# Performance work log

Hardware: AMD Instinct MI355X
Metric: run time of the kernel (lower is better)

Reference implementation:

```python
import jax, jax.numpy as jnp
import numpy as np

B, N, H = 16, 4096, 2048

def setup_inputs() -> dict:
    key = jax.random.key(0)
    k1, k2 = jax.random.split(key)
    outputs = jax.random.normal(k1, (B, N, H), dtype=jnp.float32)
    last_h = jax.random.normal(k2, (B, H), dtype=jnp.float32)
    return {"outputs": outputs, "last_h": last_h}

def reference(outputs, last_h):
    # q: [B, H] single query; k = v = outputs: [B, N, H]
    scale = jnp.asarray(outputs.shape[-1] ** 0.5, dtype=outputs.dtype)
    # logits: [B, N]
    logits = jnp.einsum("bh,bnh->bn", last_h, outputs) / scale
    attn = jax.nn.softmax(logits, axis=-1)          # [B, N]
    ctx = jnp.einsum("bn,bnh->bh", attn, outputs)   # [B, H]
    return (ctx, attn)
```

## Files before the change

### kernel.cpp

```cpp
#include <hip/hip_runtime.h>
#include <math.h>

constexpr int B = 16;
constexpr int N = 4096;
constexpr int H = 2048;

constexpr int BLOCKS_PER_BATCH = 64;
constexpr int WAVES_PER_BLOCK  = 4;
constexpr int WAVES_PER_BATCH  = BLOCKS_PER_BATCH * WAVES_PER_BLOCK;
constexpr int ROWS_PER_WAVE    = N / WAVES_PER_BATCH;
constexpr int F4_PER_ROW       = H / 4;
constexpr int F4_PER_LANE      = F4_PER_ROW / 64;

constexpr float kInvScale = 0.022097086912079608f;

__global__ __launch_bounds__(256, 4) void attn_pass1(
    const float* __restrict__ outs,
    const float* __restrict__ last_h,
    float* __restrict__ ws_logits,
    float* __restrict__ ws_m,
    float* __restrict__ ws_l,
    float* __restrict__ ws_ctx)
{
    const int b    = blockIdx.x / BLOCKS_PER_BATCH;
    const int blk  = blockIdx.x % BLOCKS_PER_BATCH;
    const int wave = threadIdx.x >> 6;
    const int lane = threadIdx.x & 63;
    const int wid  = blk * WAVES_PER_BLOCK + wave;
    const int row0 = wid * ROWS_PER_WAVE;

    const float4* q4 = reinterpret_cast<const float4*>(last_h + (size_t)b * H);
    float4 q[F4_PER_LANE];
#pragma unroll
    for (int j = 0; j < F4_PER_LANE; ++j) q[j] = q4[lane + 64 * j];

    float4 ctx[F4_PER_LANE];
#pragma unroll
    for (int j = 0; j < F4_PER_LANE; ++j) ctx[j] = make_float4(0.f, 0.f, 0.f, 0.f);
    float m = -INFINITY;
    float l = 0.f;

    const float4* krow = reinterpret_cast<const float4*>(outs) +
                         ((size_t)b * N + row0) * F4_PER_ROW;

    for (int r = 0; r < ROWS_PER_WAVE; ++r) {
        float4 k[F4_PER_LANE];
#pragma unroll
        for (int j = 0; j < F4_PER_LANE; ++j) k[j] = krow[lane + 64 * j];
        krow += F4_PER_ROW;

        float s = 0.f;
#pragma unroll
        for (int j = 0; j < F4_PER_LANE; ++j)
            s += k[j].x * q[j].x + k[j].y * q[j].y + k[j].z * q[j].z + k[j].w * q[j].w;
#pragma unroll
        for (int off = 32; off > 0; off >>= 1) s += __shfl_xor(s, off, 64);
        s *= kInvScale;

        if (lane == 0) ws_logits[(size_t)b * N + row0 + r] = s;

        if (s > m) {
            const float corr = __expf(m - s);
            l *= corr;
#pragma unroll
            for (int j = 0; j < F4_PER_LANE; ++j) {
                ctx[j].x *= corr; ctx[j].y *= corr;
                ctx[j].z *= corr; ctx[j].w *= corr;
            }
            m = s;
        }
        const float w = __expf(s - m);
        l += w;
#pragma unroll
        for (int j = 0; j < F4_PER_LANE; ++j) {
            ctx[j].x += w * k[j].x; ctx[j].y += w * k[j].y;
            ctx[j].z += w * k[j].z; ctx[j].w += w * k[j].w;
        }
    }

    const int gw = b * WAVES_PER_BATCH + wid;
    if (lane == 0) { ws_m[gw] = m; ws_l[gw] = l; }
    float4* cdst = reinterpret_cast<float4*>(ws_ctx) + (size_t)gw * F4_PER_ROW;
#pragma unroll
    for (int j = 0; j < F4_PER_LANE; ++j) cdst[lane + 64 * j] = ctx[j];
}

__global__ __launch_bounds__(256) void attn_pass2(
    const float* __restrict__ ws_logits,
    const float* __restrict__ ws_m,
    const float* __restrict__ ws_l,
    const float* __restrict__ ws_ctx,
    float* __restrict__ out_ctx,
    float* __restrict__ out_attn)
{
    __shared__ float lm[WAVES_PER_BATCH];
    __shared__ float lscale[WAVES_PER_BATCH];
    __shared__ float lsl[WAVES_PER_BATCH];
    __shared__ float4 red[128];

    const int bid  = blockIdx.x;
    const int b    = bid >> 3;
    const int part = bid & 7;
    const int tid  = threadIdx.x;

    const float mw = ws_m[b * WAVES_PER_BATCH + tid];
    const float lw = ws_l[b * WAVES_PER_BATCH + tid];
    lm[tid] = mw;
    __syncthreads();

    float M = -INFINITY;
    for (int w = 0; w < WAVES_PER_BATCH; ++w) M = fmaxf(M, lm[w]);

    const float sc = __expf(mw - M);
    lscale[tid] = sc;
    lsl[tid]    = sc * lw;
    __syncthreads();

    float L = 0.f;
    for (int w = 0; w < WAVES_PER_BATCH; ++w) L += lsl[w];
    const float invL = 1.f / L;

    if (part < 4) {
        const int f  = part * 128 + (tid & 127);
        const int wh = tid >> 7;
        const float4* c4 = reinterpret_cast<const float4*>(ws_ctx) +
                           (size_t)b * WAVES_PER_BATCH * F4_PER_ROW;
        float4 acc = make_float4(0.f, 0.f, 0.f, 0.f);
        for (int w = wh * 128; w < wh * 128 + 128; ++w) {
            const float s = lscale[w];
            const float4 v = c4[(size_t)w * F4_PER_ROW + f];
            acc.x += s * v.x; acc.y += s * v.y;
            acc.z += s * v.z; acc.w += s * v.w;
        }
        if (wh == 1) red[tid & 127] = acc;
        __syncthreads();
        if (wh == 0) {
            const float4 o = red[tid];
            float4* o4 = reinterpret_cast<float4*>(out_ctx) + (size_t)b * F4_PER_ROW;
            o4[f] = make_float4((acc.x + o.x) * invL, (acc.y + o.y) * invL,
                                (acc.z + o.z) * invL, (acc.w + o.w) * invL);
        }
    } else {
        const int n0 = (part - 4) * 1024;
#pragma unroll
        for (int i = 0; i < 4; ++i) {
            const int n = n0 + i * 256 + tid;
            out_attn[(size_t)b * N + n] =
                __expf(ws_logits[(size_t)b * N + n] - M) * invL;
        }
    }
}

extern "C" void kernel_launch(void* const* d_in, const int* in_sizes, int n_in,
                              void* d_out, int out_size, void* d_ws, size_t ws_size,
                              hipStream_t stream) {
    const float* outs   = (const float*)d_in[0];
    const float* last_h = (const float*)d_in[1];

    float* out_ctx  = (float*)d_out;
    float* out_attn = (float*)d_out + (size_t)B * H;

    float* ws        = (float*)d_ws;
    float* ws_logits = ws;
    float* ws_m      = ws_logits + (size_t)B * N;
    float* ws_l      = ws_m + (size_t)B * WAVES_PER_BATCH;
    float* ws_ctx    = ws_l + (size_t)B * WAVES_PER_BATCH;

    attn_pass1<<<B * BLOCKS_PER_BATCH, 256, 0, stream>>>(
        outs, last_h, ws_logits, ws_m, ws_l, ws_ctx);
    attn_pass2<<<B * 8, 256, 0, stream>>>(
        ws_logits, ws_m, ws_l, ws_ctx, out_ctx, out_attn);
}
```

Before: 728.8 us.

## Merge wave partials in shared memory and use nontemporal loads for keys

```diff
diff --git a/kernel.cpp b/kernel.cpp
--- a/kernel.cpp
+++ b/kernel.cpp
@@ -5,16 +5,23 @@
 constexpr int N = 4096;
 constexpr int H = 2048;
 
-constexpr int BLOCKS_PER_BATCH = 64;
+constexpr int BLOCKS_PER_BATCH = 32;
 constexpr int WAVES_PER_BLOCK  = 4;
 constexpr int WAVES_PER_BATCH  = BLOCKS_PER_BATCH * WAVES_PER_BLOCK;
 constexpr int ROWS_PER_WAVE    = N / WAVES_PER_BATCH;
 constexpr int F4_PER_ROW       = H / 4;
 constexpr int F4_PER_LANE      = F4_PER_ROW / 64;
+constexpr int PARTIALS         = BLOCKS_PER_BATCH;
 
 constexpr float kInvScale = 0.022097086912079608f;
 
-__global__ __launch_bounds__(256, 4) void attn_pass1(
+typedef float vf4 __attribute__((ext_vector_type(4)));
+
+__device__ __forceinline__ vf4 ntload(const vf4* p) {
+    return __builtin_nontemporal_load(p);
+}
+
+__global__ __launch_bounds__(256, 2) void attn_pass1(
     const float* __restrict__ outs,
     const float* __restrict__ last_h,
     float* __restrict__ ws_logits,
@@ -22,6 +29,10 @@
     float* __restrict__ ws_l,
     float* __restrict__ ws_ctx)
 {
+    __shared__ float lm[WAVES_PER_BLOCK];
+    __shared__ float ll[WAVES_PER_BLOCK];
+    __shared__ vf4   lctx[WAVES_PER_BLOCK][F4_PER_ROW];
+
     const int b    = blockIdx.x / BLOCKS_PER_BATCH;
     const int blk  = blockIdx.x % BLOCKS_PER_BATCH;
     const int wave = threadIdx.x >> 6;
@@ -29,24 +40,24 @@
     const int wid  = blk * WAVES_PER_BLOCK + wave;
     const int row0 = wid * ROWS_PER_WAVE;
 
-    const float4* q4 = reinterpret_cast<const float4*>(last_h + (size_t)b * H);
-    float4 q[F4_PER_LANE];
+    const vf4* q4 = reinterpret_cast<const vf4*>(last_h + (size_t)b * H);
+    vf4 q[F4_PER_LANE];
 #pragma unroll
     for (int j = 0; j < F4_PER_LANE; ++j) q[j] = q4[lane + 64 * j];
 
-    float4 ctx[F4_PER_LANE];
+    vf4 ctx[F4_PER_LANE];
 #pragma unroll
-    for (int j = 0; j < F4_PER_LANE; ++j) ctx[j] = make_float4(0.f, 0.f, 0.f, 0.f);
+    for (int j = 0; j < F4_PER_LANE; ++j) ctx[j] = (vf4){0.f, 0.f, 0.f, 0.f};
     float m = -INFINITY;
     float l = 0.f;
 
-    const float4* krow = reinterpret_cast<const float4*>(outs) +
-                         ((size_t)b * N + row0) * F4_PER_ROW;
+    const vf4* krow = reinterpret_cast<const vf4*>(outs) +
+                      ((size_t)b * N + row0) * F4_PER_ROW;
 
     for (int r = 0; r < ROWS_PER_WAVE; ++r) {
-        float4 k[F4_PER_LANE];
+        vf4 k[F4_PER_LANE];
 #pragma unroll
-        for (int j = 0; j < F4_PER_LANE; ++j) k[j] = krow[lane + 64 * j];
+        for (int j = 0; j < F4_PER_LANE; ++j) k[j] = ntload(&krow[lane + 64 * j]);
         krow += F4_PER_ROW;
 
         float s = 0.f;
@@ -63,26 +74,37 @@
             const float corr = __expf(m - s);
             l *= corr;
 #pragma unroll
-            for (int j = 0; j < F4_PER_LANE; ++j) {
-                ctx[j].x *= corr; ctx[j].y *= corr;
-                ctx[j].z *= corr; ctx[j].w *= corr;
-            }
+            for (int j = 0; j < F4_PER_LANE; ++j) ctx[j] *= corr;
             m = s;
         }
         const float w = __expf(s - m);
         l += w;
 #pragma unroll
-        for (int j = 0; j < F4_PER_LANE; ++j) {
-            ctx[j].x += w * k[j].x; ctx[j].y += w * k[j].y;
-            ctx[j].z += w * k[j].z; ctx[j].w += w * k[j].w;
-        }
+        for (int j = 0; j < F4_PER_LANE; ++j) ctx[j] += w * k[j];
     }
 
-    const int gw = b * WAVES_PER_BATCH + wid;
-    if (lane == 0) { ws_m[gw] = m; ws_l[gw] = l; }
-    float4* cdst = reinterpret_cast<float4*>(ws_ctx) + (size_t)gw * F4_PER_ROW;
 #pragma unroll
-    for (int j = 0; j < F4_PER_LANE; ++j) cdst[lane + 64 * j] = ctx[j];
+    for (int j = 0; j < F4_PER_LANE; ++j) lctx[wave][lane + 64 * j] = ctx[j];
+    if (lane == 0) { lm[wave] = m; ll[wave] = l; }
+    __syncthreads();
+
+    const float m0 = lm[0], m1 = lm[1], m2 = lm[2], m3 = lm[3];
+    const float Mb = fmaxf(fmaxf(m0, m1), fmaxf(m2, m3));
+    const float s0 = __expf(m0 - Mb), s1 = __expf(m1 - Mb),
+                s2 = __expf(m2 - Mb), s3 = __expf(m3 - Mb);
+    const float Lb = s0 * ll[0] + s1 * ll[1] + s2 * ll[2] + s3 * ll[3];
+
+    const int gp = b * PARTIALS + blk;
+    vf4* cdst = reinterpret_cast<vf4*>(ws_ctx) + (size_t)gp * F4_PER_ROW;
+    const int tid = threadIdx.x;
+#pragma unroll
+    for (int rep = 0; rep < 2; ++rep) {
+        const int f = tid + rep * 256;
+        const vf4 acc = s0 * lctx[0][f] + s1 * lctx[1][f] +
+                        s2 * lctx[2][f] + s3 * lctx[3][f];
+        cdst[f] = acc;
+    }
+    if (tid == 0) { ws_m[gp] = Mb; ws_l[gp] = Lb; }
 }
 
 __global__ __launch_bounds__(256) void attn_pass2(
@@ -93,52 +115,54 @@
     float* __restrict__ out_ctx,
     float* __restrict__ out_attn)
 {
-    __shared__ float lm[WAVES_PER_BATCH];
-    __shared__ float lscale[WAVES_PER_BATCH];
-    __shared__ float lsl[WAVES_PER_BATCH];
-    __shared__ float4 red[128];
+    __shared__ float lm[PARTIALS];
+    __shared__ float lscale[PARTIALS];
+    __shared__ float lsl[PARTIALS];
+    __shared__ vf4 red[128];
 
     const int bid  = blockIdx.x;
     const int b    = bid >> 3;
     const int part = bid & 7;
     const int tid  = threadIdx.x;
 
-    const float mw = ws_m[b * WAVES_PER_BATCH + tid];
-    const float lw = ws_l[b * WAVES_PER_BATCH + tid];
-    lm[tid] = mw;
+    if (tid < PARTIALS) {
+        lm[tid] = ws_m[b * PARTIALS + tid];
+    }
     __syncthreads();
 
     float M = -INFINITY;
-    for (int w = 0; w < WAVES_PER_BATCH; ++w) M = fmaxf(M, lm[w]);
+#pragma unroll
+    for (int w = 0; w < PARTIALS; ++w) M = fmaxf(M, lm[w]);
 
-    const float sc = __expf(mw - M);
-    lscale[tid] = sc;
-    lsl[tid]    = sc * lw;
+    if (tid < PARTIALS) {
+        const float sc = __expf(lm[tid] - M);
+        lscale[tid] = sc;
+        lsl[tid]    = sc * ws_l[b * PARTIALS + tid];
+    }
     __syncthreads();
 
     float L = 0.f;
-    for (int w = 0; w < WAVES_PER_BATCH; ++w) L += lsl[w];
+#pragma unroll
+    for (int w = 0; w < PARTIALS; ++w) L += lsl[w];
     const float invL = 1.f / L;
 
     if (part < 4) {
         const int f  = part * 128 + (tid & 127);
         const int wh = tid >> 7;
-        const float4* c4 = reinterpret_cast<const float4*>(ws_ctx) +
-                           (size_t)b * WAVES_PER_BATCH * F4_PER_ROW;
-        float4 acc = make_float4(0.f, 0.f, 0.f, 0.f);
-        for (int w = wh * 128; w < wh * 128 + 128; ++w) {
-            const float s = lscale[w];
-            const float4 v = c4[(size_t)w * F4_PER_ROW + f];
-            acc.x += s * v.x; acc.y += s * v.y;
-            acc.z += s * v.z; acc.w += s * v.w;
+        const vf4* c4 = reinterpret_cast<const vf4*>(ws_ctx) +
+                        (size_t)b * PARTIALS * F4_PER_ROW;
+        vf4 acc = (vf4){0.f, 0.f, 0.f, 0.f};
+#pragma unroll
+        for (int i = 0; i < 16; ++i) {
+            const int w = wh * 16 + i;
+            acc += lscale[w] * c4[(size_t)w * F4_PER_ROW + f];
         }
         if (wh == 1) red[tid & 127] = acc;
         __syncthreads();
         if (wh == 0) {
-            const float4 o = red[tid];
-            float4* o4 = reinterpret_cast<float4*>(out_ctx) + (size_t)b * F4_PER_ROW;
-            o4[f] = make_float4((acc.x + o.x) * invL, (acc.y + o.y) * invL,
-                                (acc.z + o.z) * invL, (acc.w + o.w) * invL);
+            acc += red[tid];
+            vf4* o4 = reinterpret_cast<vf4*>(out_ctx) + (size_t)b * F4_PER_ROW;
+            o4[f] = acc * invL;
         }
     } else {
         const int n0 = (part - 4) * 1024;
@@ -163,8 +187,8 @@
     float* ws        = (float*)d_ws;
     float* ws_logits = ws;
     float* ws_m      = ws_logits + (size_t)B * N;
-    float* ws_l      = ws_m + (size_t)B * WAVES_PER_BATCH;
-    float* ws_ctx    = ws_l + (size_t)B * WAVES_PER_BATCH;
+    float* ws_l      = ws_m + (size_t)B * PARTIALS;
+    float* ws_ctx    = ws_l + (size_t)B * PARTIALS;
 
     attn_pass1<<<B * BLOCKS_PER_BATCH, 256, 0, stream>>>(
         outs, last_h, ws_logits, ws_m, ws_l, ws_ctx);
```

Result: faster. 650.4 us (-10.8%).
